# Kernel optimization log

Hardware: AMD Instinct MI355X
Metric: run time of the kernel (lower is better)

## Reference

```python
import jax, jax.numpy as jnp
import numpy as np

N = 65536          # total nodes
B = 64             # graphs in batch
NPG = N // B       # nodes per graph (equal-size graphs)
K = 128            # n_clusters (assignment dim)
D_IN = 128         # node feature dim
D = 128            # pooled feature dim
E = 1048576        # edges (avg degree 16)


def setup_inputs() -> dict:
    key = jax.random.key(0)
    k1, k2, k3, k4, k5, k6 = jax.random.split(key, 6)
    h = jax.random.normal(k1, (N, D_IN), dtype=jnp.float32)
    fea = jax.random.normal(k2, (B * K, D), dtype=jnp.float32)
    W_self = jax.random.normal(k3, (D_IN, K), dtype=jnp.float32) / np.sqrt(D_IN)
    W_neigh = jax.random.normal(k4, (D_IN, K), dtype=jnp.float32) / np.sqrt(D_IN)
    b = jnp.zeros((K,), dtype=jnp.float32)
    # edges kept within each graph: sample local ids then offset by graph base
    base = jnp.repeat(jnp.arange(B, dtype=jnp.int64) * NPG, E // B)
    edge_src = jax.random.randint(k5, (E,), 0, NPG, dtype=jnp.int64) + base
    edge_dst = jax.random.randint(k6, (E,), 0, NPG, dtype=jnp.int64) + base
    return {"h": h, "fea": fea, "W_self": W_self, "W_neigh": W_neigh,
            "b": b, "edge_src": edge_src, "edge_dst": edge_dst}


def reference(h, fea, W_self, W_neigh, b, edge_src, edge_dst):
    # GraphSage mean aggregation: neigh[i] = mean_{j: (j->i)} h[j]
    deg = jnp.zeros((N,), h.dtype).at[edge_dst].add(1.0)
    neigh = jnp.zeros((N, D_IN), h.dtype).at[edge_dst].add(h[edge_src])
    neigh = neigh / jnp.maximum(deg, 1.0)[:, None]
    assign = jax.nn.relu(h @ W_self + neigh @ W_neigh + b)       # [N, K]
    assign = jax.nn.softmax(assign, axis=1)                       # softmax over clusters
    # block-diagonal mm == per-graph GEMM: [B, n, K] @ [B, K, D] -> [B, n, D]
    out = jnp.einsum('bnk,bkd->bnd',
                     assign.reshape(B, NPG, K),
                     fea.reshape(B, K, D))
    return out.reshape(N, D)
```

## Files before the change

### kernel.cpp

```cpp
#include <hip/hip_runtime.h>

#define N_NODES 65536
#define B_G     64
#define NPG     1024
#define KC      128
#define DIN     128
#define E_EDGES 1048576
#define EPG     16384
#define NSLICE  8
#define SLICE_E (EPG / NSLICE)
#define CSTRIDE (EPG + NPG)

typedef __attribute__((ext_vector_type(8))) short short8;
typedef __attribute__((ext_vector_type(4))) float floatx4;

static __device__ __forceinline__ short f2bf(float x) {
    unsigned u = __float_as_uint(x);
    unsigned r = (u + 0x7FFF + ((u >> 16) & 1)) >> 16;
    return (short)r;
}
static __device__ __forceinline__ unsigned pack2(float a, float b) {
    return (unsigned)(unsigned short)f2bf(a) | ((unsigned)(unsigned short)f2bf(b) << 16);
}

__global__ __launch_bounds__(256) void setup_a(
    const float* __restrict__ Wself, const float* __restrict__ Wneigh,
    const float* __restrict__ fea, const float* __restrict__ h,
    const int* __restrict__ edst,
    short* __restrict__ wt, short* __restrict__ feaT, short* __restrict__ h_bf,
    int* __restrict__ slicecnt)
{
    int bid = blockIdx.x;
    int tid = threadIdx.x;
    if (bid < B_G * NSLICE) {
        __shared__ int cnt[NPG];
        int g = bid >> 3, s = bid & 7;
        int gbase = g << 10;
        for (int i = tid; i < NPG; i += 256) cnt[i] = 0;
        __syncthreads();
        const int* ed = edst + (size_t)g * EPG + s * SLICE_E;
#pragma unroll
        for (int it = 0; it < SLICE_E / 256; it++)
            atomicAdd(&cnt[ed[it * 256 + tid] - gbase], 1);
        __syncthreads();
        int* sc = slicecnt + ((size_t)bid << 10);
        for (int i = tid; i < NPG; i += 256) sc[i] = cnt[i];
    } else {
        long idx = (long)(bid - B_G * NSLICE) * 256 + tid;
        if (idx < 32768) {
            int n = (int)(idx >> 8), k = (int)(idx & 255);
            float v = (k < 128) ? Wself[k * 128 + n] : Wneigh[(k - 128) * 128 + n];
            wt[idx] = f2bf(v);
        } else if (idx < 32768 + 1048576) {
            long fi = idx - 32768;
            int g = (int)(fi >> 14), d = (int)((fi >> 7) & 127), k = (int)(fi & 127);
            feaT[fi] = f2bf(fea[((long)g * 128 + k) * 128 + d]);
        } else {
            long gi = idx - 32768 - 1048576;
            const float4* hp = (const float4*)h + gi * 2;
            float4 a = hp[0], b4 = hp[1];
            uint4 w;
            w.x = pack2(a.x, a.y);
            w.y = pack2(a.z, a.w);
            w.z = pack2(b4.x, b4.y);
            w.w = pack2(b4.z, b4.w);
            ((uint4*)h_bf)[gi] = w;
        }
    }
}

__global__ __launch_bounds__(1024) void setup_b(
    const int* __restrict__ slicecnt, int* __restrict__ offs,
    int* __restrict__ deg, int* __restrict__ sliceoffs)
{
    __shared__ int sa[NPG];
    int g = blockIdx.x;
    int tid = threadIdx.x;
    int s8[NSLICE];
    int d = 0;
#pragma unroll
    for (int s = 0; s < NSLICE; s++) {
        s8[s] = slicecnt[(((size_t)g * NSLICE + s) << 10) + tid];
        d += s8[s];
    }
    int p = (d + 1) & ~1;
    sa[tid] = p;
    __syncthreads();
    for (int off = 1; off < NPG; off <<= 1) {
        int v = sa[tid];
        int vv = (tid >= off) ? sa[tid - off] : 0;
        __syncthreads();
        sa[tid] = v + vv;
        __syncthreads();
    }
    int excl = sa[tid] - p;
    offs[(g << 10) + tid] = excl;
    deg[(g << 10) + tid] = d;
    int run = excl;
#pragma unroll
    for (int s = 0; s < NSLICE; s++) {
        sliceoffs[(((size_t)g * NSLICE + s) << 10) + tid] = run;
        run += s8[s];
    }
}

__global__ __launch_bounds__(256) void setup_c(
    const int* __restrict__ esrc, const int* __restrict__ edst,
    const int* __restrict__ sliceoffs, unsigned short* __restrict__ csr)
{
    __shared__ int cur[NPG];
    int bid = blockIdx.x;
    int tid = threadIdx.x;
    int g = bid >> 3, s = bid & 7;
    int gbase = g << 10;
    const int* so = sliceoffs + ((size_t)bid << 10);
    for (int i = tid; i < NPG; i += 256) cur[i] = so[i];
    __syncthreads();
    const int* ed = edst + (size_t)g * EPG + s * SLICE_E;
    const int* es = esrc + (size_t)g * EPG + s * SLICE_E;
    unsigned short* cg = csr + (size_t)g * CSTRIDE;
#pragma unroll
    for (int it = 0; it < SLICE_E / 256; it++) {
        int e = it * 256 + tid;
        int d = ed[e] - gbase;
        int src = es[e] - gbase;
        int pos = atomicAdd(&cur[d], 1);
        cg[pos] = (unsigned short)src;
    }
}

__global__ __launch_bounds__(256) void agg_kernel(
    const short* __restrict__ h_bf, const unsigned short* __restrict__ csr,
    const int* __restrict__ offs, const int* __restrict__ deg,
    short* __restrict__ neigh)
{
    int g = blockIdx.x & 63;
    int chunk = blockIdx.x >> 6;
    int wave = threadIdx.x >> 6, lane = threadIdx.x & 63;
    int local = chunk * 4 + wave;
    int node = g * NPG + local;
    int start = offs[node];
    int m = deg[node];
    const unsigned short* lst = csr + (size_t)g * CSTRIDE + start;
    const uint2* rows = (const uint2*)h_bf + (size_t)g * NPG * 32;
    int l31 = lane & 31;
    int hi = lane >> 5;
    float s0 = 0.f, s1 = 0.f, s2 = 0.f, s3 = 0.f;
    int pairs = m >> 1;
    int p = 0;
    for (; p + 4 <= pairs; p += 4) {
        unsigned pp[4];
#pragma unroll
        for (int u = 0; u < 4; u++) pp[u] = *(const unsigned*)(lst + 2 * (p + u));
        uint2 v[4];
#pragma unroll
        for (int u = 0; u < 4; u++) {
            int s = hi ? (int)(pp[u] >> 16) : (int)(pp[u] & 0xffff);
            v[u] = rows[s * 32 + l31];
        }
#pragma unroll
        for (int u = 0; u < 4; u++) {
            s0 += __uint_as_float(v[u].x << 16);
            s1 += __uint_as_float(v[u].x & 0xffff0000u);
            s2 += __uint_as_float(v[u].y << 16);
            s3 += __uint_as_float(v[u].y & 0xffff0000u);
        }
    }
    for (; p < pairs; p++) {
        unsigned pp = *(const unsigned*)(lst + 2 * p);
        int s = hi ? (int)(pp >> 16) : (int)(pp & 0xffff);
        uint2 vv = rows[s * 32 + l31];
        s0 += __uint_as_float(vv.x << 16);
        s1 += __uint_as_float(vv.x & 0xffff0000u);
        s2 += __uint_as_float(vv.y << 16);
        s3 += __uint_as_float(vv.y & 0xffff0000u);
    }
    if (m & 1) {
        int s = lst[m - 1];
        if (!hi) {
            uint2 vv = rows[s * 32 + l31];
            s0 += __uint_as_float(vv.x << 16);
            s1 += __uint_as_float(vv.x & 0xffff0000u);
            s2 += __uint_as_float(vv.y << 16);
            s3 += __uint_as_float(vv.y & 0xffff0000u);
        }
    }
    s0 += __shfl_xor(s0, 32, 64);
    s1 += __shfl_xor(s1, 32, 64);
    s2 += __shfl_xor(s2, 32, 64);
    s3 += __shfl_xor(s3, 32, 64);
    if (!hi) {
        float invd = 1.0f / fmaxf((float)m, 1.0f);
        uint2 w;
        w.x = pack2(s0 * invd, s1 * invd);
        w.y = pack2(s2 * invd, s3 * invd);
        ((uint2*)neigh)[(size_t)node * 32 + l31] = w;
    }
}

__global__ __launch_bounds__(256) void fused_kernel(
    const short* __restrict__ h_bf, const short* __restrict__ neigh,
    const short* __restrict__ wt, const float* __restrict__ bias,
    const short* __restrict__ feaT, float* __restrict__ out)
{
    __shared__ __align__(16) char smem[50688];
    short* lds_a = (short*)smem;
    short* lds_b = lds_a + 128 * 72;
    short* ldsP  = (short*)smem;
    short* ldsB2 = ldsP + 128 * 132;

    int tid = threadIdx.x;
    int tile_m = blockIdx.x * 128;
    int g = tile_m >> 10;
    int wave = tid >> 6, lane = tid & 63;
    int l15 = lane & 15, quad = lane >> 4;

    floatx4 zz = {0.f, 0.f, 0.f, 0.f};
    floatx4 acc[2][8];
#pragma unroll
    for (int i = 0; i < 2; i++)
#pragma unroll
        for (int j = 0; j < 8; j++) acc[i][j] = zz;

    int row_s = tid >> 1;
    int c0 = (tid & 1) * 32;

    for (int kk = 0; kk < 4; kk++) {
        const short* src = (kk < 2)
            ? h_bf + (size_t)(tile_m + row_s) * DIN + kk * 64 + c0
            : neigh + (size_t)(tile_m + row_s) * DIN + (kk - 2) * 64 + c0;
        short* dsta = lds_a + row_s * 72 + c0;
#pragma unroll
        for (int i = 0; i < 32; i += 8)
            *reinterpret_cast<short8*>(dsta + i) = *reinterpret_cast<const short8*>(src + i);
        const short* srcb = wt + row_s * 256 + kk * 64 + c0;
        short* dstb = lds_b + row_s * 72 + c0;
#pragma unroll
        for (int i = 0; i < 32; i += 8)
            *reinterpret_cast<short8*>(dstb + i) = *reinterpret_cast<const short8*>(srcb + i);
        __syncthreads();
#pragma unroll
        for (int ks = 0; ks < 2; ks++) {
            short8 af[2];
#pragma unroll
            for (int rb = 0; rb < 2; rb++) {
                int m = wave * 32 + rb * 16 + l15;
                af[rb] = *reinterpret_cast<const short8*>(lds_a + m * 72 + ks * 32 + quad * 8);
            }
#pragma unroll
            for (int cb = 0; cb < 8; cb++) {
                int n = cb * 16 + l15;
                short8 bf = *reinterpret_cast<const short8*>(lds_b + n * 72 + ks * 32 + quad * 8);
                acc[0][cb] = __builtin_amdgcn_mfma_f32_16x16x32_bf16(af[0], bf, acc[0][cb], 0, 0, 0);
                acc[1][cb] = __builtin_amdgcn_mfma_f32_16x16x32_bf16(af[1], bf, acc[1][cb], 0, 0, 0);
            }
        }
        __syncthreads();
    }

    float bv[8];
#pragma unroll
    for (int cb = 0; cb < 8; cb++) bv[cb] = bias[cb * 16 + l15];

#pragma unroll
    for (int rb = 0; rb < 2; rb++) {
#pragma unroll
        for (int v = 0; v < 4; v++) {
            float x[8];
            float m = -1e30f;
#pragma unroll
            for (int cb = 0; cb < 8; cb++) {
                float t = acc[rb][cb][v] + bv[cb];
                t = fmaxf(t, 0.f);
                x[cb] = t;
                m = fmaxf(m, t);
            }
#pragma unroll
            for (int off = 1; off < 16; off <<= 1) m = fmaxf(m, __shfl_xor(m, off, 64));
            float s = 0.f;
#pragma unroll
            for (int cb = 0; cb < 8; cb++) { x[cb] = __expf(x[cb] - m); s += x[cb]; }
#pragma unroll
            for (int off = 1; off < 16; off <<= 1) s += __shfl_xor(s, off, 64);
            float inv = 1.0f / s;
            int row = wave * 32 + rb * 16 + quad * 4 + v;
#pragma unroll
            for (int cb = 0; cb < 8; cb++)
                ldsP[row * 132 + cb * 16 + l15] = f2bf(x[cb] * inv);
        }
    }

    floatx4 oacc[2][8];
#pragma unroll
    for (int i = 0; i < 2; i++)
#pragma unroll
        for (int j = 0; j < 8; j++) oacc[i][j] = zz;

    int r2 = tid >> 2;
    int c2 = (tid & 3) * 32;
    short8 pf[2][4];

    for (int half = 0; half < 2; half++) {
        if (half) __syncthreads();
        const short* srcb = feaT + ((size_t)g * 128 + half * 64 + r2) * 128 + c2;
        short* dstb = ldsB2 + r2 * 132 + c2;
#pragma unroll
        for (int i = 0; i < 32; i += 8)
            *reinterpret_cast<short8*>(dstb + i) = *reinterpret_cast<const short8*>(srcb + i);
        __syncthreads();
        if (half == 0) {
#pragma unroll
            for (int rb = 0; rb < 2; rb++)
#pragma unroll
                for (int ks = 0; ks < 4; ks++)
                    pf[rb][ks] = *reinterpret_cast<const short8*>(
                        ldsP + (wave * 32 + rb * 16 + l15) * 132 + ks * 32 + quad * 8);
        }
#pragma unroll
        for (int cb2 = 0; cb2 < 4; cb2++) {
            int cb = half * 4 + cb2;
#pragma unroll
            for (int ks = 0; ks < 4; ks++) {
                short8 bf = *reinterpret_cast<const short8*>(
                    ldsB2 + (cb2 * 16 + l15) * 132 + ks * 32 + quad * 8);
                oacc[0][cb] = __builtin_amdgcn_mfma_f32_16x16x32_bf16(pf[0][ks], bf, oacc[0][cb], 0, 0, 0);
                oacc[1][cb] = __builtin_amdgcn_mfma_f32_16x16x32_bf16(pf[1][ks], bf, oacc[1][cb], 0, 0, 0);
            }
        }
    }

#pragma unroll
    for (int rb = 0; rb < 2; rb++)
#pragma unroll
        for (int v = 0; v < 4; v++) {
            int row = tile_m + wave * 32 + rb * 16 + quad * 4 + v;
#pragma unroll
            for (int cb = 0; cb < 8; cb++)
                out[(size_t)row * 128 + cb * 16 + l15] = oacc[rb][cb][v];
        }
}

extern "C" void kernel_launch(void* const* d_in, const int* in_sizes, int n_in,
                              void* d_out, int out_size, void* d_ws, size_t ws_size,
                              hipStream_t stream) {
    const float* h      = (const float*)d_in[0];
    const float* fea    = (const float*)d_in[1];
    const float* Wself  = (const float*)d_in[2];
    const float* Wneigh = (const float*)d_in[3];
    const float* bias   = (const float*)d_in[4];
    const int*   esrc   = (const int*)d_in[5];
    const int*   edst   = (const int*)d_in[6];
    float* out = (float*)d_out;

    char* ws = (char*)d_ws;
    short* h_bf = (short*)ws;
    size_t off = (size_t)N_NODES * DIN * sizeof(short);
    short* neigh = (short*)(ws + off); off += (size_t)N_NODES * DIN * sizeof(short);
    short* wt    = (short*)(ws + off); off += (size_t)128 * 256 * sizeof(short);
    short* feaT  = (short*)(ws + off); off += (size_t)B_G * 128 * 128 * sizeof(short);
    unsigned short* csr = (unsigned short*)(ws + off); off += (size_t)B_G * CSTRIDE * sizeof(short);
    int* offs = (int*)(ws + off); off += (size_t)N_NODES * sizeof(int);
    int* deg  = (int*)(ws + off); off += (size_t)N_NODES * sizeof(int);
    int* slicecnt  = (int*)(ws + off); off += (size_t)B_G * NSLICE * NPG * sizeof(int);
    int* sliceoffs = (int*)(ws + off);

    setup_a<<<B_G * NSLICE + 8320, 256, 0, stream>>>(Wself, Wneigh, fea, h, edst,
                                                     wt, feaT, h_bf, slicecnt);
    setup_b<<<B_G, 1024, 0, stream>>>(slicecnt, offs, deg, sliceoffs);
    setup_c<<<B_G * NSLICE, 256, 0, stream>>>(esrc, edst, sliceoffs, csr);
    agg_kernel<<<256 * B_G, 256, 0, stream>>>(h_bf, csr, offs, deg, neigh);
    fused_kernel<<<N_NODES / 128, 256, 0, stream>>>(h_bf, neigh, wt, bias, feaT, out);
}
```

Before: 174.9 us.

## Fuse CSR build (count, scan, scatter) into one block per graph

The three setup kernels (per-slice degree counting, prefix scan, slice scatter) are merged into a single kernel in which one block per graph counts degrees, scans offsets in shared memory and scatters source ids into the CSR. This removes two kernel launches and the global slicecnt/sliceoffs round trips. The trade-off is that only 64 blocks now do the edge work instead of 512, so each block runs a longer serial loop over 16K edges and parallelism drops. That work does overlap with the conversion blocks in the same launch.

```diff
diff --git a/kernel.cpp b/kernel.cpp
--- a/kernel.cpp
+++ b/kernel.cpp
@@ -7,8 +7,6 @@
 #define DIN     128
 #define E_EDGES 1048576
 #define EPG     16384
-#define NSLICE  8
-#define SLICE_E (EPG / NSLICE)
 #define CSTRIDE (EPG + NPG)
 
 typedef __attribute__((ext_vector_type(8))) short short8;
@@ -23,30 +21,67 @@
     return (unsigned)(unsigned short)f2bf(a) | ((unsigned)(unsigned short)f2bf(b) << 16);
 }
 
-__global__ __launch_bounds__(256) void setup_a(
+__global__ __launch_bounds__(256) void setup_all(
     const float* __restrict__ Wself, const float* __restrict__ Wneigh,
     const float* __restrict__ fea, const float* __restrict__ h,
-    const int* __restrict__ edst,
+    const int* __restrict__ esrc, const int* __restrict__ edst,
     short* __restrict__ wt, short* __restrict__ feaT, short* __restrict__ h_bf,
-    int* __restrict__ slicecnt)
+    int* __restrict__ offs, int* __restrict__ deg, unsigned short* __restrict__ csr)
 {
     int bid = blockIdx.x;
     int tid = threadIdx.x;
-    if (bid < B_G * NSLICE) {
+    if (bid < B_G) {
         __shared__ int cnt[NPG];
-        int g = bid >> 3, s = bid & 7;
+        __shared__ int cur[NPG];
+        __shared__ int sc[256];
+        int g = bid;
         int gbase = g << 10;
         for (int i = tid; i < NPG; i += 256) cnt[i] = 0;
         __syncthreads();
-        const int* ed = edst + (size_t)g * EPG + s * SLICE_E;
-#pragma unroll
-        for (int it = 0; it < SLICE_E / 256; it++)
+        const int* ed = edst + (size_t)g * EPG;
+        const int* es = esrc + (size_t)g * EPG;
+#pragma unroll 4
+        for (int it = 0; it < EPG / 256; it++)
             atomicAdd(&cnt[ed[it * 256 + tid] - gbase], 1);
         __syncthreads();
-        int* sc = slicecnt + ((size_t)bid << 10);
-        for (int i = tid; i < NPG; i += 256) sc[i] = cnt[i];
+        int c[4], p[4];
+        int local = 0;
+#pragma unroll
+        for (int i = 0; i < 4; i++) {
+            c[i] = cnt[tid * 4 + i];
+            p[i] = (c[i] + 1) & ~1;
+            local += p[i];
+        }
+        sc[tid] = local;
+        __syncthreads();
+        for (int off = 1; off < 256; off <<= 1) {
+            int v = sc[tid];
+            int vv = (tid >= off) ? sc[tid - off] : 0;
+            __syncthreads();
+            sc[tid] = v + vv;
+            __syncthreads();
+        }
+        int run = sc[tid] - local;
+#pragma unroll
+        for (int i = 0; i < 4; i++) {
+            int node = gbase + tid * 4 + i;
+            offs[node] = run;
+            deg[node] = c[i];
+            cur[tid * 4 + i] = run;
+            run += p[i];
+        }
+        __syncthreads();
+        unsigned short* cg = csr + (size_t)g * CSTRIDE;
+#pragma unroll 4
+        for (int it = 0; it < EPG / 256; it++) {
+            int e = it * 256 + tid;
+            int d = ed[e] - gbase;
+            int s = es[e] - gbase;
+            int pos = atomicAdd(&cur[d], 1);
+            cg[pos] = (unsigned short)s;
+        }
     } else {
-        long idx = (long)(bid - B_G * NSLICE) * 256 + tid;
+        long idx = (long)(bid - B_G) * 256 + tid;
         if (idx < 32768) {
             int n = (int)(idx >> 8), k = (int)(idx & 255);
             float v = (k < 128) ? Wself[k * 128 + n] : Wneigh[(k - 128) * 128 + n];
@@ -66,66 +101,6 @@
             w.w = pack2(b4.z, b4.w);
             ((uint4*)h_bf)[gi] = w;
         }
-    }
-}
-
-__global__ __launch_bounds__(1024) void setup_b(
-    const int* __restrict__ slicecnt, int* __restrict__ offs,
-    int* __restrict__ deg, int* __restrict__ sliceoffs)
-{
-    __shared__ int sa[NPG];
-    int g = blockIdx.x;
-    int tid = threadIdx.x;
-    int s8[NSLICE];
-    int d = 0;
-#pragma unroll
-    for (int s = 0; s < NSLICE; s++) {
-        s8[s] = slicecnt[(((size_t)g * NSLICE + s) << 10) + tid];
-        d += s8[s];
-    }
-    int p = (d + 1) & ~1;
-    sa[tid] = p;
-    __syncthreads();
-    for (int off = 1; off < NPG; off <<= 1) {
-        int v = sa[tid];
-        int vv = (tid >= off) ? sa[tid - off] : 0;
-        __syncthreads();
-        sa[tid] = v + vv;
-        __syncthreads();
-    }
-    int excl = sa[tid] - p;
-    offs[(g << 10) + tid] = excl;
-    deg[(g << 10) + tid] = d;
-    int run = excl;
-#pragma unroll
-    for (int s = 0; s < NSLICE; s++) {
-        sliceoffs[(((size_t)g * NSLICE + s) << 10) + tid] = run;
-        run += s8[s];
-    }
-}
-
-__global__ __launch_bounds__(256) void setup_c(
-    const int* __restrict__ esrc, const int* __restrict__ edst,
-    const int* __restrict__ sliceoffs, unsigned short* __restrict__ csr)
-{
-    __shared__ int cur[NPG];
-    int bid = blockIdx.x;
-    int tid = threadIdx.x;
-    int g = bid >> 3, s = bid & 7;
-    int gbase = g << 10;
-    const int* so = sliceoffs + ((size_t)bid << 10);
-    for (int i = tid; i < NPG; i += 256) cur[i] = so[i];
-    __syncthreads();
-    const int* ed = edst + (size_t)g * EPG + s * SLICE_E;
-    const int* es = esrc + (size_t)g * EPG + s * SLICE_E;
-    unsigned short* cg = csr + (size_t)g * CSTRIDE;
-#pragma unroll
-    for (int it = 0; it < SLICE_E / 256; it++) {
-        int e = it * 256 + tid;
-        int d = ed[e] - gbase;
-        int src = es[e] - gbase;
-        int pos = atomicAdd(&cur[d], 1);
-        cg[pos] = (unsigned short)src;
     }
 }
 
@@ -360,14 +335,10 @@
     short* feaT  = (short*)(ws + off); off += (size_t)B_G * 128 * 128 * sizeof(short);
     unsigned short* csr = (unsigned short*)(ws + off); off += (size_t)B_G * CSTRIDE * sizeof(short);
     int* offs = (int*)(ws + off); off += (size_t)N_NODES * sizeof(int);
-    int* deg  = (int*)(ws + off); off += (size_t)N_NODES * sizeof(int);
-    int* slicecnt  = (int*)(ws + off); off += (size_t)B_G * NSLICE * NPG * sizeof(int);
-    int* sliceoffs = (int*)(ws + off);
-
-    setup_a<<<B_G * NSLICE + 8320, 256, 0, stream>>>(Wself, Wneigh, fea, h, edst,
-                                                     wt, feaT, h_bf, slicecnt);
-    setup_b<<<B_G, 1024, 0, stream>>>(slicecnt, offs, deg, sliceoffs);
-    setup_c<<<B_G * NSLICE, 256, 0, stream>>>(esrc, edst, sliceoffs, csr);
+    int* deg  = (int*)(ws + off);
+
+    setup_all<<<B_G + 8320, 256, 0, stream>>>(Wself, Wneigh, fea, h, esrc, edst,
+                                              wt, feaT, h_bf, offs, deg, csr);
     agg_kernel<<<256 * B_G, 256, 0, stream>>>(h_bf, csr, offs, deg, neigh);
     fused_kernel<<<N_NODES / 128, 256, 0, stream>>>(h_bf, neigh, wt, bias, feaT, out);
 }
```

After: 193.7 us. 1.11x slower.

## Fuse neighbor mean aggregation into the GEMM kernel via LDS

Applied to the files above, without the earlier changes.

Moves the CSR gather-and-mean aggregation into the fused GEMM/softmax kernel, so each block computes its 128 nodes' neighbor means directly into shared memory. This drops the separate aggregation launch and the global write and re-read of the bf16 neighbor matrix. In exchange, parallelism for the gather phase falls from 16384 blocks to 512 blocks, each wave looping over 32 nodes serially. LDS use also grows to about 69 KB per block, which may lower occupancy and latency hiding for the random gathers.

```diff
diff --git a/kernel.cpp b/kernel.cpp
--- a/kernel.cpp
+++ b/kernel.cpp
@@ -129,91 +129,89 @@
     }
 }
 
-__global__ __launch_bounds__(256) void agg_kernel(
+__global__ __launch_bounds__(256) void fused_kernel(
     const short* __restrict__ h_bf, const unsigned short* __restrict__ csr,
     const int* __restrict__ offs, const int* __restrict__ deg,
-    short* __restrict__ neigh)
-{
-    int g = blockIdx.x & 63;
-    int chunk = blockIdx.x >> 6;
-    int wave = threadIdx.x >> 6, lane = threadIdx.x & 63;
-    int local = chunk * 4 + wave;
-    int node = g * NPG + local;
-    int start = offs[node];
-    int m = deg[node];
-    const unsigned short* lst = csr + (size_t)g * CSTRIDE + start;
-    const uint2* rows = (const uint2*)h_bf + (size_t)g * NPG * 32;
-    int l31 = lane & 31;
-    int hi = lane >> 5;
-    float s0 = 0.f, s1 = 0.f, s2 = 0.f, s3 = 0.f;
-    int pairs = m >> 1;
-    int p = 0;
-    for (; p + 4 <= pairs; p += 4) {
-        unsigned pp[4];
-#pragma unroll
-        for (int u = 0; u < 4; u++) pp[u] = *(const unsigned*)(lst + 2 * (p + u));
-        uint2 v[4];
-#pragma unroll
-        for (int u = 0; u < 4; u++) {
-            int s = hi ? (int)(pp[u] >> 16) : (int)(pp[u] & 0xffff);
-            v[u] = rows[s * 32 + l31];
-        }
-#pragma unroll
-        for (int u = 0; u < 4; u++) {
-            s0 += __uint_as_float(v[u].x << 16);
-            s1 += __uint_as_float(v[u].x & 0xffff0000u);
-            s2 += __uint_as_float(v[u].y << 16);
-            s3 += __uint_as_float(v[u].y & 0xffff0000u);
-        }
-    }
-    for (; p < pairs; p++) {
-        unsigned pp = *(const unsigned*)(lst + 2 * p);
-        int s = hi ? (int)(pp >> 16) : (int)(pp & 0xffff);
-        uint2 vv = rows[s * 32 + l31];
-        s0 += __uint_as_float(vv.x << 16);
-        s1 += __uint_as_float(vv.x & 0xffff0000u);
-        s2 += __uint_as_float(vv.y << 16);
-        s3 += __uint_as_float(vv.y & 0xffff0000u);
-    }
-    if (m & 1) {
-        int s = lst[m - 1];
-        if (!hi) {
-            uint2 vv = rows[s * 32 + l31];
-            s0 += __uint_as_float(vv.x << 16);
-            s1 += __uint_as_float(vv.x & 0xffff0000u);
-            s2 += __uint_as_float(vv.y << 16);
-            s3 += __uint_as_float(vv.y & 0xffff0000u);
-        }
-    }
-    s0 += __shfl_xor(s0, 32, 64);
-    s1 += __shfl_xor(s1, 32, 64);
-    s2 += __shfl_xor(s2, 32, 64);
-    s3 += __shfl_xor(s3, 32, 64);
-    if (!hi) {
-        float invd = 1.0f / fmaxf((float)m, 1.0f);
-        uint2 w;
-        w.x = pack2(s0 * invd, s1 * invd);
-        w.y = pack2(s2 * invd, s3 * invd);
-        ((uint2*)neigh)[(size_t)node * 32 + l31] = w;
-    }
-}
-
-__global__ __launch_bounds__(256) void fused_kernel(
-    const short* __restrict__ h_bf, const short* __restrict__ neigh,
     const short* __restrict__ wt, const float* __restrict__ bias,
     const short* __restrict__ feaT, float* __restrict__ out)
 {
-    __shared__ __align__(16) char smem[50688];
-    short* lds_a = (short*)smem;
+    __shared__ __align__(16) char smem[70656];
+    short* ldsN  = (short*)smem;
+    short* ldsP  = ldsN;
+    short* lds_a = ldsN + 128 * 132;
     short* lds_b = lds_a + 128 * 72;
-    short* ldsP  = (short*)smem;
-    short* ldsB2 = ldsP + 128 * 132;
+    short* ldsB2 = lds_a;
 
     int tid = threadIdx.x;
     int tile_m = blockIdx.x * 128;
     int g = tile_m >> 10;
     int wave = tid >> 6, lane = tid & 63;
     int l15 = lane & 15, quad = lane >> 4;
+    int l31 = lane & 31, hi = lane >> 5;
+
+    {
+        const uint2* rows = (const uint2*)h_bf + (size_t)g * NPG * 32;
+        const unsigned short* cbase = csr + (size_t)g * CSTRIDE;
+        for (int n = 0; n < 32; n++) {
+            int lr = wave * 32 + n;
+            int node = tile_m + lr;
+            int start = offs[node];
+            int m = deg[node];
+            const unsigned short* lst = cbase + start;
+            float s0 = 0.f, s1 = 0.f, s2 = 0.f, s3 = 0.f;
+            int pairs = m >> 1;
+            int p = 0;
+            for (; p + 4 <= pairs; p += 4) {
+                unsigned pp[4];
+#pragma unroll
+                for (int u = 0; u < 4; u++) pp[u] = *(const unsigned*)(lst + 2 * (p + u));
+                uint2 v[4];
+#pragma unroll
+                for (int u = 0; u < 4; u++) {
+                    int s = hi ? (int)(pp[u] >> 16) : (int)(pp[u] & 0xffff);
+                    v[u] = rows[s * 32 + l31];
+                }
+#pragma unroll
+                for (int u = 0; u < 4; u++) {
+                    s0 += __uint_as_float(v[u].x << 16);
+                    s1 += __uint_as_float(v[u].x & 0xffff0000u);
+                    s2 += __uint_as_float(v[u].y << 16);
+                    s3 += __uint_as_float(v[u].y & 0xffff0000u);
+                }
+            }
+            for (; p < pairs; p++) {
+                unsigned pp = *(const unsigned*)(lst + 2 * p);
+                int s = hi ? (int)(pp >> 16) : (int)(pp & 0xffff);
+                uint2 vv = rows[s * 32 + l31];
+                s0 += __uint_as_float(vv.x << 16);
+                s1 += __uint_as_float(vv.x & 0xffff0000u);
+                s2 += __uint_as_float(vv.y << 16);
+                s3 += __uint_as_float(vv.y & 0xffff0000u);
+            }
+            if (m & 1) {
+                int s = lst[m - 1];
+                if (!hi) {
+                    uint2 vv = rows[s * 32 + l31];
+                    s0 += __uint_as_float(vv.x << 16);
+                    s1 += __uint_as_float(vv.x & 0xffff0000u);
+                    s2 += __uint_as_float(vv.y << 16);
+                    s3 += __uint_as_float(vv.y & 0xffff0000u);
+                }
+            }
+            s0 += __shfl_xor(s0, 32, 64);
+            s1 += __shfl_xor(s1, 32, 64);
+            s2 += __shfl_xor(s2, 32, 64);
+            s3 += __shfl_xor(s3, 32, 64);
+            if (!hi) {
+                float invd = 1.0f / fmaxf((float)m, 1.0f);
+                uint2 w2;
+                w2.x = pack2(s0 * invd, s1 * invd);
+                w2.y = pack2(s2 * invd, s3 * invd);
+                *(uint2*)(ldsN + lr * 132 + l31 * 4) = w2;
+            }
+        }
+    }
+    __syncthreads();
 
     floatx4 zz = {0.f, 0.f, 0.f, 0.f};
     floatx4 acc[2][8];
@@ -226,13 +224,13 @@
     int c0 = (tid & 1) * 32;
 
     for (int kk = 0; kk < 4; kk++) {
-        const short* src = (kk < 2)
-            ? h_bf + (size_t)(tile_m + row_s) * DIN + kk * 64 + c0
-            : neigh + (size_t)(tile_m + row_s) * DIN + (kk - 2) * 64 + c0;
-        short* dsta = lds_a + row_s * 72 + c0;
-#pragma unroll
-        for (int i = 0; i < 32; i += 8)
-            *reinterpret_cast<short8*>(dsta + i) = *reinterpret_cast<const short8*>(src + i);
+        if (kk < 2) {
+            const short* src = h_bf + (size_t)(tile_m + row_s) * DIN + kk * 64 + c0;
+            short* dsta = lds_a + row_s * 72 + c0;
+#pragma unroll
+            for (int i = 0; i < 32; i += 8)
+                *reinterpret_cast<short8*>(dsta + i) = *reinterpret_cast<const short8*>(src + i);
+        }
         const short* srcb = wt + row_s * 256 + kk * 64 + c0;
         short* dstb = lds_b + row_s * 72 + c0;
 #pragma unroll
@@ -245,7 +243,9 @@
 #pragma unroll
             for (int rb = 0; rb < 2; rb++) {
                 int m = wave * 32 + rb * 16 + l15;
-                af[rb] = *reinterpret_cast<const short8*>(lds_a + m * 72 + ks * 32 + quad * 8);
+                af[rb] = (kk < 2)
+                    ? *reinterpret_cast<const short8*>(lds_a + m * 72 + ks * 32 + quad * 8)
+                    : *reinterpret_cast<const short8*>(ldsN + m * 132 + (kk - 2) * 64 + ks * 32 + quad * 8);
             }
 #pragma unroll
             for (int cb = 0; cb < 8; cb++) {
@@ -355,7 +355,6 @@
     char* ws = (char*)d_ws;
     short* h_bf = (short*)ws;
     size_t off = (size_t)N_NODES * DIN * sizeof(short);
-    short* neigh = (short*)(ws + off); off += (size_t)N_NODES * DIN * sizeof(short);
     short* wt    = (short*)(ws + off); off += (size_t)128 * 256 * sizeof(short);
     short* feaT  = (short*)(ws + off); off += (size_t)B_G * 128 * 128 * sizeof(short);
     unsigned short* csr = (unsigned short*)(ws + off); off += (size_t)B_G * CSTRIDE * sizeof(short);
@@ -368,6 +367,5 @@
                                                      wt, feaT, h_bf, slicecnt);
     setup_b<<<B_G, 1024, 0, stream>>>(slicecnt, offs, deg, sliceoffs);
     setup_c<<<B_G * NSLICE, 256, 0, stream>>>(esrc, edst, sliceoffs, csr);
-    agg_kernel<<<256 * B_G, 256, 0, stream>>>(h_bf, csr, offs, deg, neigh);
-    fused_kernel<<<N_NODES / 128, 256, 0, stream>>>(h_bf, neigh, wt, bias, feaT, out);
-}
+    fused_kernel<<<N_NODES / 128, 256, 0, stream>>>(h_bf, csr, offs, deg, wt, bias, feaT, out);
+}
```

New measurement: 299.0 us. 1.71x slower.

## Load GEMM operands directly from global memory and regroup aggregation blocks by graph

Applied to the files above, without the earlier changes.

The fused kernel stops staging the A/B GEMM tiles and the fea tile through shared memory. Each wave now reads its MFMA fragments straight from global memory (through the caches), which removes most __syncthreads and shrinks LDS to the softmax P buffer alone. The aggregation kernel's block-to-graph mapping is switched so consecutive blocks work on the same graph, which should improve cache locality for gathers of neighbour rows. The trade-off is redundant global/L2 traffic, since several waves load the same weight fragments in uncoalesced 16-byte pieces. The P buffer is synchronised only with an lgkmcnt wait inside each wave, which holds only because each wave reads back just the rows it wrote.

```diff
diff --git a/kernel.cpp b/kernel.cpp
--- a/kernel.cpp
+++ b/kernel.cpp
@@ -134,8 +134,8 @@
     const int* __restrict__ offs, const int* __restrict__ deg,
     short* __restrict__ neigh)
 {
-    int g = blockIdx.x & 63;
-    int chunk = blockIdx.x >> 6;
+    int g = blockIdx.x >> 8;
+    int chunk = blockIdx.x & 255;
     int wave = threadIdx.x >> 6, lane = threadIdx.x & 63;
     int local = chunk * 4 + wave;
     int node = g * NPG + local;
@@ -203,11 +203,7 @@
     const short* __restrict__ wt, const float* __restrict__ bias,
     const short* __restrict__ feaT, float* __restrict__ out)
 {
-    __shared__ __align__(16) char smem[50688];
-    short* lds_a = (short*)smem;
-    short* lds_b = lds_a + 128 * 72;
-    short* ldsP  = (short*)smem;
-    short* ldsB2 = ldsP + 128 * 132;
+    __shared__ __align__(16) short ldsP[128 * 132];
 
     int tid = threadIdx.x;
     int tile_m = blockIdx.x * 128;
@@ -222,40 +218,27 @@
 #pragma unroll
         for (int j = 0; j < 8; j++) acc[i][j] = zz;
 
-    int row_s = tid >> 1;
-    int c0 = (tid & 1) * 32;
-
+#pragma unroll
     for (int kk = 0; kk < 4; kk++) {
-        const short* src = (kk < 2)
-            ? h_bf + (size_t)(tile_m + row_s) * DIN + kk * 64 + c0
-            : neigh + (size_t)(tile_m + row_s) * DIN + (kk - 2) * 64 + c0;
-        short* dsta = lds_a + row_s * 72 + c0;
-#pragma unroll
-        for (int i = 0; i < 32; i += 8)
-            *reinterpret_cast<short8*>(dsta + i) = *reinterpret_cast<const short8*>(src + i);
-        const short* srcb = wt + row_s * 256 + kk * 64 + c0;
-        short* dstb = lds_b + row_s * 72 + c0;
-#pragma unroll
-        for (int i = 0; i < 32; i += 8)
-            *reinterpret_cast<short8*>(dstb + i) = *reinterpret_cast<const short8*>(srcb + i);
-        __syncthreads();
 #pragma unroll
         for (int ks = 0; ks < 2; ks++) {
+            int colk = kk * 64 + ks * 32 + quad * 8;
             short8 af[2];
 #pragma unroll
             for (int rb = 0; rb < 2; rb++) {
-                int m = wave * 32 + rb * 16 + l15;
-                af[rb] = *reinterpret_cast<const short8*>(lds_a + m * 72 + ks * 32 + quad * 8);
+                int m = tile_m + wave * 32 + rb * 16 + l15;
+                af[rb] = (kk < 2)
+                    ? *reinterpret_cast<const short8*>(h_bf + (size_t)m * DIN + colk)
+                    : *reinterpret_cast<const short8*>(neigh + (size_t)m * DIN + (colk - 128));
             }
 #pragma unroll
             for (int cb = 0; cb < 8; cb++) {
                 int n = cb * 16 + l15;
-                short8 bf = *reinterpret_cast<const short8*>(lds_b + n * 72 + ks * 32 + quad * 8);
+                short8 bf = *reinterpret_cast<const short8*>(wt + n * 256 + colk);
                 acc[0][cb] = __builtin_amdgcn_mfma_f32_16x16x32_bf16(af[0], bf, acc[0][cb], 0, 0, 0);
                 acc[1][cb] = __builtin_amdgcn_mfma_f32_16x16x32_bf16(af[1], bf, acc[1][cb], 0, 0, 0);
             }
         }
-        __syncthreads();
     }
 
     float bv[8];
@@ -290,42 +273,30 @@
         }
     }
 
+    asm volatile("s_waitcnt lgkmcnt(0)" ::: "memory");
+
     floatx4 oacc[2][8];
 #pragma unroll
     for (int i = 0; i < 2; i++)
 #pragma unroll
         for (int j = 0; j < 8; j++) oacc[i][j] = zz;
 
-    int r2 = tid >> 2;
-    int c2 = (tid & 3) * 32;
     short8 pf[2][4];
-
-    for (int half = 0; half < 2; half++) {
-        if (half) __syncthreads();
-        const short* srcb = feaT + ((size_t)g * 128 + half * 64 + r2) * 128 + c2;
-        short* dstb = ldsB2 + r2 * 132 + c2;
-#pragma unroll
-        for (int i = 0; i < 32; i += 8)
-            *reinterpret_cast<short8*>(dstb + i) = *reinterpret_cast<const short8*>(srcb + i);
-        __syncthreads();
-        if (half == 0) {
-#pragma unroll
-            for (int rb = 0; rb < 2; rb++)
-#pragma unroll
-                for (int ks = 0; ks < 4; ks++)
-                    pf[rb][ks] = *reinterpret_cast<const short8*>(
-                        ldsP + (wave * 32 + rb * 16 + l15) * 132 + ks * 32 + quad * 8);
-        }
-#pragma unroll
-        for (int cb2 = 0; cb2 < 4; cb2++) {
-            int cb = half * 4 + cb2;
-#pragma unroll
-            for (int ks = 0; ks < 4; ks++) {
-                short8 bf = *reinterpret_cast<const short8*>(
-                    ldsB2 + (cb2 * 16 + l15) * 132 + ks * 32 + quad * 8);
-                oacc[0][cb] = __builtin_amdgcn_mfma_f32_16x16x32_bf16(pf[0][ks], bf, oacc[0][cb], 0, 0, 0);
-                oacc[1][cb] = __builtin_amdgcn_mfma_f32_16x16x32_bf16(pf[1][ks], bf, oacc[1][cb], 0, 0, 0);
-            }
+#pragma unroll
+    for (int rb = 0; rb < 2; rb++)
+#pragma unroll
+        for (int ks = 0; ks < 4; ks++)
+            pf[rb][ks] = *reinterpret_cast<const short8*>(
+                ldsP + (wave * 32 + rb * 16 + l15) * 132 + ks * 32 + quad * 8);
+
+#pragma unroll
+    for (int cb = 0; cb < 8; cb++) {
+#pragma unroll
+        for (int ks = 0; ks < 4; ks++) {
+            short8 bf = *reinterpret_cast<const short8*>(
+                feaT + ((size_t)g * 128 + cb * 16 + l15) * 128 + ks * 32 + quad * 8);
+            oacc[0][cb] = __builtin_amdgcn_mfma_f32_16x16x32_bf16(pf[0][ks], bf, oacc[0][cb], 0, 0, 0);
+            oacc[1][cb] = __builtin_amdgcn_mfma_f32_16x16x32_bf16(pf[1][ks], bf, oacc[1][cb], 0, 0, 0);
         }
     }
 
```

After: 187.9 us. 1.07x slower.
